# Optimization experiments

Hardware: AMD Instinct MI355X
Metric: run time of the kernel (lower is better)

## Reference

```python
import jax, jax.numpy as jnp
import numpy as np

TEMPERATURE = 8.0  # sqrt(d_k), d_k = 64


def setup_inputs() -> dict:
    key = jax.random.key(0)
    kq, kk, kv = jax.random.split(key, 3)
    BH, N, D = 16, 4096, 64  # batch*heads, seq_len, head_dim
    q = jax.random.normal(kq, (BH, N, D), dtype=jnp.float32)
    k = jax.random.normal(kk, (BH, N, D), dtype=jnp.float32)
    v = jax.random.normal(kv, (BH, N, D), dtype=jnp.float32)
    # causal mask: True means masked (filled with -inf), broadcast over BH
    mask = jnp.triu(jnp.ones((N, N), dtype=jnp.bool_), k=1)[None, :, :]
    return {"q": q, "k": k, "v": v, "mask": mask}


def reference(q, k, v, mask):
    # attn = q @ k^T / temperature, masked softmax, attn @ v
    scores = jnp.einsum("bnd,bmd->bnm", q, k) / TEMPERATURE
    scores = jnp.where(mask, -jnp.inf, scores)
    attn = jax.nn.softmax(scores, axis=-1)  # dropout p=0 (eval) -> identity
    out = jnp.einsum("bnm,bmd->bnd", attn, v)
    return out, attn
```

## Files before the change

kernel.cpp:

```cpp
#include <hip/hip_runtime.h>

typedef float f32x4 __attribute__((ext_vector_type(4)));
typedef __bf16 bf16x8 __attribute__((ext_vector_type(8)));
typedef unsigned short u16x8 __attribute__((ext_vector_type(8)));

#define NBH 16
#define NSEQ 4096
#define DH 64

__device__ __forceinline__ unsigned int cvtpk(float lo, float hi) {
  unsigned int r;
  asm("v_cvt_pk_bf16_f32 %0, %1, %2" : "=v"(r) : "v"(lo), "v"(hi));
  return r;
}
__device__ __forceinline__ bf16x8 pk8(const float* f) {
  union { unsigned int u[4]; bf16x8 b; } x;
#pragma unroll
  for (int i = 0; i < 4; ++i) x.u[i] = cvtpk(f[2 * i], f[2 * i + 1]);
  return x.b;
}

__global__ __launch_bounds__(256, 4) void lsum_kernel(
    const float* __restrict__ qg, const float* __restrict__ kg, float* __restrict__ lsum) {
  const int bid = blockIdx.x;
  const int kk = bid >> 3;
  const int b = 2 * (bid & 7) + (kk >> 6);
  const int tt = kk & 63;
  const int qt = (tt < 32) ? (63 - tt) : (tt - 32);

  const int tid = threadIdx.x;
  const int w = tid >> 6, lane = tid & 63;
  const int g = lane >> 4, c = lane & 15;
  const int qr0 = qt * 64, wr0 = 16 * w;

  const float* qb = qg + (size_t)b * NSEQ * DH;
  const float* kb = kg + (size_t)b * NSEQ * DH;

  __shared__ unsigned short Kl[2][64][72];

  bf16x8 aq[2];
  {
    const float* qrow = qb + (size_t)(qr0 + wr0 + c) * DH;
#pragma unroll
    for (int ks = 0; ks < 2; ++ks) {
      float f[8];
      *(float4*)f = *(const float4*)(qrow + 32 * ks + 8 * g);
      *(float4*)(f + 4) = *(const float4*)(qrow + 32 * ks + 8 * g + 4);
      aq[ks] = pk8(f);
    }
  }

  const int kj = tid >> 2, kcs = tid & 3;
  float kf[16];
  auto loadK = [&](int kt) {
    const float* src = kb + (size_t)(kt * 64 + kj) * DH + kcs * 16;
#pragma unroll
    for (int i = 0; i < 4; ++i) *(float4*)(kf + 4 * i) = ((const float4*)src)[i];
  };
  auto writeK = [&](int cur) {
    unsigned int* dst = (unsigned int*)&Kl[cur][kj][kcs * 16];
#pragma unroll
    for (int i = 0; i < 8; ++i) dst[i] = cvtpk(kf[2 * i], kf[2 * i + 1]);
  };

  loadK(0);
  float part[4] = {0.f, 0.f, 0.f, 0.f};
  for (int kt = 0; kt <= qt; ++kt) {
    const int cur = kt & 1;
    writeK(cur);
    __syncthreads();
    if (kt < qt) loadK(kt + 1);
    f32x4 acc[4];
#pragma unroll
    for (int ct = 0; ct < 4; ++ct) acc[ct] = (f32x4){0.f, 0.f, 0.f, 0.f};
#pragma unroll
    for (int ks = 0; ks < 2; ++ks)
#pragma unroll
      for (int ct = 0; ct < 4; ++ct) {
        u16x8 u = *(const u16x8*)&Kl[cur][16 * ct + c][32 * ks + 8 * g];
        acc[ct] = __builtin_amdgcn_mfma_f32_16x16x32_bf16(aq[ks], __builtin_bit_cast(bf16x8, u), acc[ct], 0, 0, 0);
      }
    const bool diag = (kt == qt);
#pragma unroll
    for (int ct = 0; ct < 4; ++ct)
#pragma unroll
      for (int r = 0; r < 4; ++r) {
        float s = acc[ct][r] * 0.125f;
        int j = kt * 64 + 16 * ct + c;
        int i = qr0 + wr0 + 4 * g + r;
        part[r] += (!diag || j <= i) ? __expf(s) : 0.f;
      }
  }
#pragma unroll
  for (int r = 0; r < 4; ++r) {
    float s = part[r];
    s += __shfl_xor(s, 1); s += __shfl_xor(s, 2);
    s += __shfl_xor(s, 4); s += __shfl_xor(s, 8);
    if (c == 0) lsum[(size_t)b * NSEQ + qr0 + wr0 + 4 * g + r] = s;
  }
}

__global__ __launch_bounds__(256, 4) void attn_kernel(
    const float* __restrict__ qg, const float* __restrict__ kg,
    const float* __restrict__ vg, const float* __restrict__ lsum,
    float* __restrict__ outg) {
  const int bid = blockIdx.x;
  const int kk = bid >> 3;
  const int b = 2 * (bid & 7) + (kk >> 6);
  const int tt = kk & 63;
  const int qt = (tt < 32) ? (63 - tt) : (tt - 32);

  const int tid = threadIdx.x;
  const int w = tid >> 6, lane = tid & 63;
  const int g = lane >> 4, c = lane & 15;
  const int qr0 = qt * 64, wr0 = 16 * w;

  const float* qb = qg + (size_t)b * NSEQ * DH;
  const float* kb = kg + (size_t)b * NSEQ * DH;
  const float* vb = vg + (size_t)b * NSEQ * DH;
  float* outb = outg + (size_t)b * NSEQ * DH;
  float* attnb = outg + (size_t)NBH * NSEQ * DH + (size_t)b * NSEQ * NSEQ;

  __shared__ unsigned short Kl[2][64][72];
  __shared__ unsigned int Vt[2][64][37];

  float rinv[4];
#pragma unroll
  for (int r = 0; r < 4; ++r) rinv[r] = 1.f / lsum[(size_t)b * NSEQ + qr0 + wr0 + 4 * g + r];

  bf16x8 aq[2];
  {
    const float* qrow = qb + (size_t)(qr0 + wr0 + c) * DH;
#pragma unroll
    for (int ks = 0; ks < 2; ++ks) {
      float f[8];
      *(float4*)f = *(const float4*)(qrow + 32 * ks + 8 * g);
      *(float4*)(f + 4) = *(const float4*)(qrow + 32 * ks + 8 * g + 4);
      aq[ks] = pk8(f);
    }
  }

  const int kj = tid >> 2, kcs = tid & 3;
  const int vp = tid >> 3, vch = tid & 7;
  float kf[16], vf0[8], vf1[8];

  auto loadK = [&](int kt) {
    const float* src = kb + (size_t)(kt * 64 + kj) * DH + kcs * 16;
#pragma unroll
    for (int i = 0; i < 4; ++i) *(float4*)(kf + 4 * i) = ((const float4*)src)[i];
  };
  auto loadV = [&](int kt) {
    const float* s0 = vb + (size_t)(kt * 64 + 2 * vp) * DH + vch * 8;
    *(float4*)vf0 = ((const float4*)s0)[0];
    *(float4*)(vf0 + 4) = ((const float4*)s0)[1];
    const float* s1 = s0 + DH;
    *(float4*)vf1 = ((const float4*)s1)[0];
    *(float4*)(vf1 + 4) = ((const float4*)s1)[1];
  };
  auto writeK = [&](int cur) {
    unsigned int* dst = (unsigned int*)&Kl[cur][kj][kcs * 16];
#pragma unroll
    for (int i = 0; i < 8; ++i) dst[i] = cvtpk(kf[2 * i], kf[2 * i + 1]);
  };
  auto writeV = [&](int cur) {
#pragma unroll
    for (int e = 0; e < 8; ++e) Vt[cur][vch * 8 + e][vp] = cvtpk(vf0[e], vf1[e]);
  };

  loadK(0);
  loadV(0);

  f32x4 oacc[4];
#pragma unroll
  for (int ct = 0; ct < 4; ++ct) oacc[ct] = (f32x4){0.f, 0.f, 0.f, 0.f};

  for (int kt = 0; kt <= qt; ++kt) {
    const int cur = kt & 1;
    writeK(cur);
    writeV(cur);
    __syncthreads();
    if (kt < qt) { loadK(kt + 1); loadV(kt + 1); }

    f32x4 acc[4];
#pragma unroll
    for (int ct = 0; ct < 4; ++ct) acc[ct] = (f32x4){0.f, 0.f, 0.f, 0.f};
#pragma unroll
    for (int ks = 0; ks < 2; ++ks)
#pragma unroll
      for (int ct = 0; ct < 4; ++ct) {
        u16x8 u = *(const u16x8*)&Kl[cur][16 * ct + c][32 * ks + 8 * g];
        acc[ct] = __builtin_amdgcn_mfma_f32_16x16x32_bf16(aq[ks], __builtin_bit_cast(bf16x8, u), acc[ct], 0, 0, 0);
      }

    const bool diag = (kt == qt);
    unsigned short* Pl = &Kl[1 - cur][0][0];
    float prow[16];
#pragma unroll
    for (int ct = 0; ct < 4; ++ct)
#pragma unroll
      for (int r = 0; r < 4; ++r) {
        const int il = wr0 + 4 * g + r;
        const int jl = 16 * ct + c;
        float s = acc[ct][r] * 0.125f;
        float p = (!diag || (kt * 64 + jl) <= (qr0 + il)) ? __expf(s) * rinv[r] : 0.f;
        prow[4 * ct + r] = p;
        Pl[il * 72 + jl] = (unsigned short)cvtpk(p, p);
      }
    __syncthreads();

    bf16x8 ap[2];
#pragma unroll
    for (int ks = 0; ks < 2; ++ks)
      ap[ks] = __builtin_bit_cast(bf16x8, *(const u16x8*)&Pl[(wr0 + c) * 72 + 32 * ks + 8 * g]);
#pragma unroll
    for (int ks = 0; ks < 2; ++ks)
#pragma unroll
      for (int ct = 0; ct < 4; ++ct) {
        u16x8 bv = *(const u16x8*)&Vt[cur][16 * ct + c][16 * ks + 4 * g];
        oacc[ct] = __builtin_amdgcn_mfma_f32_16x16x32_bf16(ap[ks], __builtin_bit_cast(bf16x8, bv), oacc[ct], 0, 0, 0);
      }

#pragma unroll
    for (int ct = 0; ct < 4; ++ct)
#pragma unroll
      for (int r = 0; r < 4; ++r) {
        const int i = qr0 + wr0 + 4 * g + r;
        attnb[(size_t)i * NSEQ + kt * 64 + 16 * ct + c] = prow[4 * ct + r];
      }
    __syncthreads();
  }

#pragma unroll
  for (int ct = 0; ct < 4; ++ct)
#pragma unroll
    for (int r = 0; r < 4; ++r) {
      const int i = qr0 + wr0 + 4 * g + r;
      outb[(size_t)i * DH + 16 * ct + c] = oacc[ct][r];
    }

  const int zc0 = (qt + 1) * 64;
  if (zc0 < NSEQ) {
    const int zw4 = (NSEQ - zc0) >> 2;
    const float4 z = {0.f, 0.f, 0.f, 0.f};
    for (int r = 0; r < 64; ++r) {
      float4* dst = (float4*)(attnb + (size_t)(qr0 + r) * NSEQ + zc0);
      for (int c4 = tid; c4 < zw4; c4 += 256) dst[c4] = z;
    }
  }
}

extern "C" void kernel_launch(void* const* d_in, const int* in_sizes, int n_in,
                              void* d_out, int out_size, void* d_ws, size_t ws_size,
                              hipStream_t stream) {
  (void)in_sizes; (void)n_in; (void)out_size; (void)ws_size;
  const float* q = (const float*)d_in[0];
  const float* k = (const float*)d_in[1];
  const float* v = (const float*)d_in[2];
  float* out = (float*)d_out;
  float* lsum = (float*)d_ws;
  lsum_kernel<<<dim3(1024), dim3(256), 0, stream>>>(q, k, lsum);
  attn_kernel<<<dim3(1024), dim3(256), 0, stream>>>(q, k, v, lsum, out);
}
```

Before: 352.9 us.

## Fuse row-sum and attention passes into one kernel with 128-row tiles

Merges the separate row-sum kernel and attention kernel into one launch. Each block now holds 128 query rows across 8 waves, computes the softmax denominators in a first pass over K, then runs the P and PV pass. A dedicated P buffer in shared memory removes two barriers per iteration. This drops the workspace round trip and a launch, and halves redundant K/V loads per query row. In exchange there are half as many blocks (512), each with a larger causal tail, so load balance may suffer.

```diff
diff --git a/kernel.cpp b/kernel.cpp
--- a/kernel.cpp
+++ b/kernel.cpp
@@ -3,6 +3,7 @@
 typedef float f32x4 __attribute__((ext_vector_type(4)));
 typedef __bf16 bf16x8 __attribute__((ext_vector_type(8)));
 typedef unsigned short u16x8 __attribute__((ext_vector_type(8)));
+typedef unsigned int u32x4 __attribute__((ext_vector_type(4)));
 
 #define NBH 16
 #define NSEQ 4096
@@ -20,23 +21,33 @@
   return x.b;
 }
 
-__global__ __launch_bounds__(256, 4) void lsum_kernel(
-    const float* __restrict__ qg, const float* __restrict__ kg, float* __restrict__ lsum) {
+__global__ __launch_bounds__(512, 4) void sdpa_fused(
+    const float* __restrict__ qg, const float* __restrict__ kg,
+    const float* __restrict__ vg, float* __restrict__ outg) {
   const int bid = blockIdx.x;
-  const int kk = bid >> 3;
-  const int b = 2 * (bid & 7) + (kk >> 6);
-  const int tt = kk & 63;
-  const int qt = (tt < 32) ? (63 - tt) : (tt - 32);
+  const int xcd = bid & 7;
+  const int idx = bid >> 3;
+  const int hh = idx >> 5;
+  const int b = 2 * xcd + hh;
+  const int tt = idx & 31;
+  const int qt2 = hh ? tt : (31 - tt);
+  const int qr0 = qt2 * 128;
+  const int nkt = 2 * (qt2 + 1);
 
   const int tid = threadIdx.x;
   const int w = tid >> 6, lane = tid & 63;
   const int g = lane >> 4, c = lane & 15;
-  const int qr0 = qt * 64, wr0 = 16 * w;
+  const int wr0 = 16 * w;
 
   const float* qb = qg + (size_t)b * NSEQ * DH;
   const float* kb = kg + (size_t)b * NSEQ * DH;
+  const float* vb = vg + (size_t)b * NSEQ * DH;
+  float* outb = outg + (size_t)b * NSEQ * DH;
+  float* attnb = outg + (size_t)NBH * NSEQ * DH + (size_t)b * NSEQ * NSEQ;
 
   __shared__ unsigned short Kl[2][64][72];
+  __shared__ unsigned int Vt[2][64][37];
+  __shared__ unsigned short Pl[128][72];
 
   bf16x8 aq[2];
   {
@@ -50,26 +61,38 @@
     }
   }
 
-  const int kj = tid >> 2, kcs = tid & 3;
-  float kf[16];
+  const int kj = tid >> 3, kcs = tid & 7;
+  const int vp = tid >> 4, dch = tid & 15;
+  float kf[8], vf0[4], vf1[4];
+
   auto loadK = [&](int kt) {
-    const float* src = kb + (size_t)(kt * 64 + kj) * DH + kcs * 16;
-#pragma unroll
-    for (int i = 0; i < 4; ++i) *(float4*)(kf + 4 * i) = ((const float4*)src)[i];
+    const float* s = kb + (size_t)(kt * 64 + kj) * DH + kcs * 8;
+    *(float4*)kf = ((const float4*)s)[0];
+    *(float4*)(kf + 4) = ((const float4*)s)[1];
   };
   auto writeK = [&](int cur) {
-    unsigned int* dst = (unsigned int*)&Kl[cur][kj][kcs * 16];
-#pragma unroll
-    for (int i = 0; i < 8; ++i) dst[i] = cvtpk(kf[2 * i], kf[2 * i + 1]);
-  };
-
+    u32x4 u;
+#pragma unroll
+    for (int i = 0; i < 4; ++i) u[i] = cvtpk(kf[2 * i], kf[2 * i + 1]);
+    *(u32x4*)&Kl[cur][kj][kcs * 8] = u;
+  };
+  auto loadV = [&](int kt) {
+    const float* s0 = vb + (size_t)(kt * 64 + 2 * vp) * DH + dch * 4;
+    *(float4*)vf0 = *(const float4*)s0;
+    *(float4*)vf1 = *(const float4*)(s0 + DH);
+  };
+  auto writeV = [&](int cur) {
+#pragma unroll
+    for (int e = 0; e < 4; ++e) Vt[cur][4 * dch + e][vp] = cvtpk(vf0[e], vf1[e]);
+  };
+
+  float part[4] = {0.f, 0.f, 0.f, 0.f};
   loadK(0);
-  float part[4] = {0.f, 0.f, 0.f, 0.f};
-  for (int kt = 0; kt <= qt; ++kt) {
+  for (int kt = 0; kt < nkt; ++kt) {
     const int cur = kt & 1;
     writeK(cur);
     __syncthreads();
-    if (kt < qt) loadK(kt + 1);
+    if (kt + 1 < nkt) loadK(kt + 1);
     f32x4 acc[4];
 #pragma unroll
     for (int ct = 0; ct < 4; ++ct) acc[ct] = (f32x4){0.f, 0.f, 0.f, 0.f};
@@ -80,106 +103,36 @@
         u16x8 u = *(const u16x8*)&Kl[cur][16 * ct + c][32 * ks + 8 * g];
         acc[ct] = __builtin_amdgcn_mfma_f32_16x16x32_bf16(aq[ks], __builtin_bit_cast(bf16x8, u), acc[ct], 0, 0, 0);
       }
-    const bool diag = (kt == qt);
 #pragma unroll
     for (int ct = 0; ct < 4; ++ct)
 #pragma unroll
       for (int r = 0; r < 4; ++r) {
-        float s = acc[ct][r] * 0.125f;
-        int j = kt * 64 + 16 * ct + c;
-        int i = qr0 + wr0 + 4 * g + r;
-        part[r] += (!diag || j <= i) ? __expf(s) : 0.f;
-      }
-  }
+        const int j = kt * 64 + 16 * ct + c;
+        const int i = qr0 + wr0 + 4 * g + r;
+        part[r] += (j <= i) ? __expf(acc[ct][r] * 0.125f) : 0.f;
+      }
+  }
+  float rinv[4];
 #pragma unroll
   for (int r = 0; r < 4; ++r) {
     float s = part[r];
     s += __shfl_xor(s, 1); s += __shfl_xor(s, 2);
     s += __shfl_xor(s, 4); s += __shfl_xor(s, 8);
-    if (c == 0) lsum[(size_t)b * NSEQ + qr0 + wr0 + 4 * g + r] = s;
-  }
-}
-
-__global__ __launch_bounds__(256, 4) void attn_kernel(
-    const float* __restrict__ qg, const float* __restrict__ kg,
-    const float* __restrict__ vg, const float* __restrict__ lsum,
-    float* __restrict__ outg) {
-  const int bid = blockIdx.x;
-  const int kk = bid >> 3;
-  const int b = 2 * (bid & 7) + (kk >> 6);
-  const int tt = kk & 63;
-  const int qt = (tt < 32) ? (63 - tt) : (tt - 32);
-
-  const int tid = threadIdx.x;
-  const int w = tid >> 6, lane = tid & 63;
-  const int g = lane >> 4, c = lane & 15;
-  const int qr0 = qt * 64, wr0 = 16 * w;
-
-  const float* qb = qg + (size_t)b * NSEQ * DH;
-  const float* kb = kg + (size_t)b * NSEQ * DH;
-  const float* vb = vg + (size_t)b * NSEQ * DH;
-  float* outb = outg + (size_t)b * NSEQ * DH;
-  float* attnb = outg + (size_t)NBH * NSEQ * DH + (size_t)b * NSEQ * NSEQ;
-
-  __shared__ unsigned short Kl[2][64][72];
-  __shared__ unsigned int Vt[2][64][37];
-
-  float rinv[4];
-#pragma unroll
-  for (int r = 0; r < 4; ++r) rinv[r] = 1.f / lsum[(size_t)b * NSEQ + qr0 + wr0 + 4 * g + r];
-
-  bf16x8 aq[2];
-  {
-    const float* qrow = qb + (size_t)(qr0 + wr0 + c) * DH;
-#pragma unroll
-    for (int ks = 0; ks < 2; ++ks) {
-      float f[8];
-      *(float4*)f = *(const float4*)(qrow + 32 * ks + 8 * g);
-      *(float4*)(f + 4) = *(const float4*)(qrow + 32 * ks + 8 * g + 4);
-      aq[ks] = pk8(f);
-    }
-  }
-
-  const int kj = tid >> 2, kcs = tid & 3;
-  const int vp = tid >> 3, vch = tid & 7;
-  float kf[16], vf0[8], vf1[8];
-
-  auto loadK = [&](int kt) {
-    const float* src = kb + (size_t)(kt * 64 + kj) * DH + kcs * 16;
-#pragma unroll
-    for (int i = 0; i < 4; ++i) *(float4*)(kf + 4 * i) = ((const float4*)src)[i];
-  };
-  auto loadV = [&](int kt) {
-    const float* s0 = vb + (size_t)(kt * 64 + 2 * vp) * DH + vch * 8;
-    *(float4*)vf0 = ((const float4*)s0)[0];
-    *(float4*)(vf0 + 4) = ((const float4*)s0)[1];
-    const float* s1 = s0 + DH;
-    *(float4*)vf1 = ((const float4*)s1)[0];
-    *(float4*)(vf1 + 4) = ((const float4*)s1)[1];
-  };
-  auto writeK = [&](int cur) {
-    unsigned int* dst = (unsigned int*)&Kl[cur][kj][kcs * 16];
-#pragma unroll
-    for (int i = 0; i < 8; ++i) dst[i] = cvtpk(kf[2 * i], kf[2 * i + 1]);
-  };
-  auto writeV = [&](int cur) {
-#pragma unroll
-    for (int e = 0; e < 8; ++e) Vt[cur][vch * 8 + e][vp] = cvtpk(vf0[e], vf1[e]);
-  };
+    rinv[r] = 1.f / s;
+  }
 
   loadK(0);
   loadV(0);
-
   f32x4 oacc[4];
 #pragma unroll
   for (int ct = 0; ct < 4; ++ct) oacc[ct] = (f32x4){0.f, 0.f, 0.f, 0.f};
 
-  for (int kt = 0; kt <= qt; ++kt) {
+  for (int kt = 0; kt < nkt; ++kt) {
     const int cur = kt & 1;
     writeK(cur);
     writeV(cur);
     __syncthreads();
-    if (kt < qt) { loadK(kt + 1); loadV(kt + 1); }
+    if (kt + 1 < nkt) { loadK(kt + 1); loadV(kt + 1); }
 
     f32x4 acc[4];
 #pragma unroll
@@ -192,26 +145,23 @@
         acc[ct] = __builtin_amdgcn_mfma_f32_16x16x32_bf16(aq[ks], __builtin_bit_cast(bf16x8, u), acc[ct], 0, 0, 0);
       }
 
-    const bool diag = (kt == qt);
-    unsigned short* Pl = &Kl[1 - cur][0][0];
-    float prow[16];
 #pragma unroll
     for (int ct = 0; ct < 4; ++ct)
 #pragma unroll
       for (int r = 0; r < 4; ++r) {
         const int il = wr0 + 4 * g + r;
         const int jl = 16 * ct + c;
-        float s = acc[ct][r] * 0.125f;
-        float p = (!diag || (kt * 64 + jl) <= (qr0 + il)) ? __expf(s) * rinv[r] : 0.f;
-        prow[4 * ct + r] = p;
-        Pl[il * 72 + jl] = (unsigned short)cvtpk(p, p);
-      }
-    __syncthreads();
+        const int i = qr0 + il;
+        const int j = kt * 64 + jl;
+        const float p = (j <= i) ? __expf(acc[ct][r] * 0.125f) * rinv[r] : 0.f;
+        Pl[il][jl] = (unsigned short)cvtpk(p, p);
+        attnb[(size_t)i * NSEQ + j] = p;
+      }
 
     bf16x8 ap[2];
 #pragma unroll
     for (int ks = 0; ks < 2; ++ks)
-      ap[ks] = __builtin_bit_cast(bf16x8, *(const u16x8*)&Pl[(wr0 + c) * 72 + 32 * ks + 8 * g]);
+      ap[ks] = __builtin_bit_cast(bf16x8, *(const u16x8*)&Pl[wr0 + c][32 * ks + 8 * g]);
 #pragma unroll
     for (int ks = 0; ks < 2; ++ks)
 #pragma unroll
@@ -219,15 +169,6 @@
         u16x8 bv = *(const u16x8*)&Vt[cur][16 * ct + c][16 * ks + 4 * g];
         oacc[ct] = __builtin_amdgcn_mfma_f32_16x16x32_bf16(ap[ks], __builtin_bit_cast(bf16x8, bv), oacc[ct], 0, 0, 0);
       }
-
-#pragma unroll
-    for (int ct = 0; ct < 4; ++ct)
-#pragma unroll
-      for (int r = 0; r < 4; ++r) {
-        const int i = qr0 + wr0 + 4 * g + r;
-        attnb[(size_t)i * NSEQ + kt * 64 + 16 * ct + c] = prow[4 * ct + r];
-      }
-    __syncthreads();
   }
 
 #pragma unroll
@@ -238,13 +179,13 @@
       outb[(size_t)i * DH + 16 * ct + c] = oacc[ct][r];
     }
 
-  const int zc0 = (qt + 1) * 64;
+  const int zc0 = 128 * (qt2 + 1);
   if (zc0 < NSEQ) {
     const int zw4 = (NSEQ - zc0) >> 2;
     const float4 z = {0.f, 0.f, 0.f, 0.f};
-    for (int r = 0; r < 64; ++r) {
+    for (int r = 0; r < 128; ++r) {
       float4* dst = (float4*)(attnb + (size_t)(qr0 + r) * NSEQ + zc0);
-      for (int c4 = tid; c4 < zw4; c4 += 256) dst[c4] = z;
+      for (int c4 = tid; c4 < zw4; c4 += 512) dst[c4] = z;
     }
   }
 }
@@ -252,12 +193,10 @@
 extern "C" void kernel_launch(void* const* d_in, const int* in_sizes, int n_in,
                               void* d_out, int out_size, void* d_ws, size_t ws_size,
                               hipStream_t stream) {
-  (void)in_sizes; (void)n_in; (void)out_size; (void)ws_size;
+  (void)in_sizes; (void)n_in; (void)out_size; (void)d_ws; (void)ws_size;
   const float* q = (const float*)d_in[0];
   const float* k = (const float*)d_in[1];
   const float* v = (const float*)d_in[2];
   float* out = (float*)d_out;
-  float* lsum = (float*)d_ws;
-  lsum_kernel<<<dim3(1024), dim3(256), 0, stream>>>(q, k, lsum);
-  attn_kernel<<<dim3(1024), dim3(256), 0, stream>>>(q, k, v, lsum, out);
-}
+  sdpa_fused<<<dim3(512), dim3(512), 0, stream>>>(q, k, v, out);
+}
```

After: 330.6 us. 6.3% less time.
